# Kernel tuning notes

Measured on AMD Instinct MI355X. Metric: run time of the kernel, lower is better.

The kernel has to match this reference:

```python
import jax, jax.numpy as jnp
import numpy as np

N = 50000      # n_nodes
E = 800000     # n_edges
IN_NF = 64     # in_node_nf
HID = 128      # hidden_nf
OUT_NF = 64    # out_node_nf
L = 4          # n_layers
EH = HID // 2  # edge MLP hidden width (edge_nf_ratio=2)
C = 1.0        # aggregation scaling constant


def _w(k, shape):
    # fan-in scaled init (matches nn.Linear scale roughly)
    return jax.random.normal(k, shape, dtype=jnp.float32) / np.sqrt(shape[-2]).astype(np.float32)


def setup_inputs() -> dict:
    key = jax.random.key(0)
    ks = jax.random.split(key, 10)
    h = jax.random.normal(ks[0], (N, IN_NF), dtype=jnp.float32)
    edges = jax.random.randint(ks[1], (2, E), 0, N, dtype=jnp.int32)
    return {
        "h": h,
        "edges": edges,
        "W_in": _w(ks[2], (IN_NF, HID)),
        "b_in": jnp.zeros((HID,), jnp.float32),
        # stacked per-layer GCL params, leading dim L
        "eW1": _w(ks[3], (L, 2 * HID, EH)),
        "eb1": jnp.zeros((L, EH), jnp.float32),
        "eW2": _w(ks[4], (L, EH, EH)),
        "eb2": jnp.zeros((L, EH), jnp.float32),
        "nW1": _w(ks[5], (L, HID + EH, HID)),
        "nb1": jnp.zeros((L, HID), jnp.float32),
        "nW2": _w(ks[6], (L, HID, HID)),
        "nb2": jnp.zeros((L, HID), jnp.float32),
        "W_out": _w(ks[7], (HID, OUT_NF)),
        "b_out": jnp.zeros((OUT_NF,), jnp.float32),
    }


def reference(h, edges, W_in, b_in, eW1, eb1, eW2, eb2, nW1, nb1, nW2, nb2, W_out, b_out):
    row, col = edges[0], edges[1]
    h = h @ W_in + b_in  # [N, HID] embedding_in

    def layer(hc, p):
        w1, b1, w2, b2, m1, c1, m2, c2 = p
        # edge model: gather endpoints, concat, 2-layer SiLU MLP
        m = jnp.concatenate([hc[row], hc[col]], axis=1)          # [E, 2*HID]
        m = jax.nn.silu(m @ w1 + b1)                             # [E, EH]
        m = jax.nn.silu(m @ w2 + b2)                             # [E, EH]
        # node model: scatter-sum messages to source nodes, scale by C
        agg = jax.ops.segment_sum(m, row, num_segments=N) * C    # [N, EH]
        z = jnp.concatenate([hc, agg], axis=1)                   # [N, HID+EH]
        z = jax.nn.silu(z @ m1 + c1)
        z = z @ m2 + c2                                          # [N, HID]
        return hc + z, None  # residual=True

    h, _ = jax.lax.scan(layer, h, (eW1, eb1, eW2, eb2, nW1, nb1, nW2, nb2))
    return h @ W_out + b_out  # [N, OUT_NF] embedding_out
```

## Files before the change

### kernel.cpp

```cpp
#include <hip/hip_runtime.h>
#include <hip/hip_bf16.h>
#include <cstdint>
#include <cstddef>

#define N_NODES 50000
#define N_EDGES 800000
#define NR      50048
#define NBKT    196
#define BSH     8
#define BCHUNK  2048
#define CAP     6144

typedef __attribute__((ext_vector_type(8))) short short8;
typedef __attribute__((ext_vector_type(4))) float floatx4;
typedef __attribute__((ext_vector_type(4))) unsigned int uintx4;

__device__ inline float bf2f(unsigned short u) {
    union { unsigned int i; float f; } v; v.i = ((unsigned int)u) << 16; return v.f;
}
__device__ inline unsigned short f2bf(float f) {
    union { float f; unsigned int i; } v; v.f = f;
    unsigned int u = v.i;
    return (unsigned short)((u + 0x7FFFu + ((u >> 16) & 1u)) >> 16);
}
__device__ inline unsigned int f2bf_pk(float a, float b) {
    __hip_bfloat162 h2 = __float22bfloat162_rn(make_float2(a, b));
    return *reinterpret_cast<unsigned int*>(&h2);
}
__device__ inline float2 bf2f2(unsigned int u) {
    union { unsigned int i; float f; } lo, hi;
    lo.i = u << 16;
    hi.i = u & 0xFFFF0000u;
    return make_float2(lo.f, hi.f);
}
__device__ inline float silu_f(float x) {
    float e = __expf(-x);
    return x * __builtin_amdgcn_rcpf(1.0f + e);
}

__device__ inline int block_excl_scan_256(int v, int* buf) {
    int tid = threadIdx.x;
    buf[tid] = v;
    __syncthreads();
    #pragma unroll
    for (int off = 1; off < 256; off <<= 1) {
        int t = (tid >= off) ? buf[tid - off] : 0;
        __syncthreads();
        buf[tid] += t;
        __syncthreads();
    }
    return buf[tid] - v;
}

__device__ inline void pack_std(const float* __restrict__ src,
                                unsigned short* __restrict__ dst,
                                int NOUT, long j) {
    int i = (int)(j & 7);
    long rest = j >> 3;
    int n = (int)(rest % NOUT);
    int kb = (int)(rest / NOUT);
    dst[j] = f2bf(src[(long)(kb * 8 + i) * NOUT + n]);
}

#define NH0   (N_NODES * 64L)
#define SW_IN 8192L
#define SW_OUT 8192L
#define SW1   16384L
#define SE2   4096L
#define SN1   24576L
#define SN2   16384L
#define SB    128L
#define PERL  (SW1 + SE2 + SN1 + SN2 + SB)
#define PACK_TOTAL (NH0 + SW_IN + SW_OUT + 4 * PERL)

__global__ __launch_bounds__(256) void pack_kernel(
    const float* __restrict__ h0, const float* __restrict__ W_in,
    const float* __restrict__ W_out, const float* __restrict__ eW1,
    const float* __restrict__ eb1, const float* __restrict__ eW2,
    const float* __restrict__ nW1, const float* __restrict__ nW2,
    unsigned short* __restrict__ h0bf, unsigned short* __restrict__ Winp,
    unsigned short* __restrict__ Woutp, unsigned short* __restrict__ W1p,
    unsigned short* __restrict__ eW2p, unsigned short* __restrict__ nW1p,
    unsigned short* __restrict__ nW2p, float* __restrict__ biasP)
{
    long idx = (long)blockIdx.x * 256 + threadIdx.x;
    if (idx >= PACK_TOTAL) return;
    long j = idx;
    if (j < NH0) { h0bf[j] = f2bf(h0[j]); return; }
    j -= NH0;
    if (j < SW_IN) { pack_std(W_in, Winp, 128, j); return; }
    j -= SW_IN;
    if (j < SW_OUT) { pack_std(W_out, Woutp, 64, j); return; }
    j -= SW_OUT;
    int l = (int)(j / PERL);
    long r = j % PERL;
    if (r < SW1) {
        int i = (int)(r & 7);
        int n = (int)((r >> 3) & 127);
        int kb = (int)(r >> 10);
        int k = kb * 8 + i;
        const float* w = eW1 + (long)l * 256 * 64;
        float v = (n < 64) ? w[(long)k * 64 + n] : w[(long)(128 + k) * 64 + (n - 64)];
        W1p[(long)l * SW1 + r] = f2bf(v);
        return;
    }
    r -= SW1;
    if (r < SE2) { pack_std(eW2 + (long)l * 4096, eW2p + (long)l * SE2, 64, r); return; }
    r -= SE2;
    if (r < SN1) { pack_std(nW1 + (long)l * 24576, nW1p + (long)l * SN1, 128, r); return; }
    r -= SN1;
    if (r < SN2) { pack_std(nW2 + (long)l * 16384, nW2p + (long)l * SN2, 128, r); return; }
    r -= SN2;
    biasP[(long)l * 128 + r] = (r < 64) ? eb1[(long)l * 64 + r] : 0.0f;
}

__global__ __launch_bounds__(256) void hist_k(const int* __restrict__ erow,
                                              int* __restrict__ countB, int E) {
    __shared__ int c[NBKT];
    for (int i = threadIdx.x; i < NBKT; i += 256) c[i] = 0;
    __syncthreads();
    int j = blockIdx.x * BCHUNK + threadIdx.x;
    #pragma unroll
    for (int i = 0; i < BCHUNK / 256; i++, j += 256)
        if (j < E) atomicAdd(&c[erow[j] >> BSH], 1);
    __syncthreads();
    for (int i = threadIdx.x; i < NBKT; i += 256)
        if (c[i]) atomicAdd(&countB[i], c[i]);
}

__global__ __launch_bounds__(256) void bucket_scan_k(const int* __restrict__ countB,
                                                     int* __restrict__ bucketBase,
                                                     int* __restrict__ bucketCursor) {
    __shared__ int buf[256];
    int tid = threadIdx.x;
    int v = (tid < NBKT) ? countB[tid] : 0;
    int excl = block_excl_scan_256(v, buf);
    if (tid < NBKT) {
        bucketBase[tid] = excl;
        bucketCursor[tid] = excl;
    }
    if (tid == NBKT - 1) bucketBase[NBKT] = excl + v;
}

__global__ __launch_bounds__(256) void bin_k(
    const int* __restrict__ erow, const int* __restrict__ ecol,
    int* __restrict__ bucketCursor, int2* __restrict__ binned, int E)
{
    __shared__ int2 staged[BCHUNK];
    __shared__ int cnt[NBKT];
    __shared__ int binStart[NBKT];
    __shared__ int gbase[NBKT];
    __shared__ int scanbuf[256];
    const int tid = threadIdx.x;
    const int base = blockIdx.x * BCHUNK;
    const int nloc = min(BCHUNK, E - base);

    for (int i = tid; i < NBKT; i += 256) cnt[i] = 0;
    __syncthreads();

    int2 ed[BCHUNK / 256];
    int  bo[BCHUNK / 256];
    #pragma unroll
    for (int i = 0; i < BCHUNK / 256; i++) {
        int jl = i * 256 + tid;
        if (jl < nloc) {
            int j = base + jl;
            int r = erow[j], c = ecol[j];
            ed[i] = make_int2(r, c);
            int b = r >> BSH;
            int off = atomicAdd(&cnt[b], 1);
            bo[i] = (b << 12) | off;
        } else bo[i] = -1;
    }
    __syncthreads();

    int v = (tid < NBKT) ? cnt[tid] : 0;
    int excl = block_excl_scan_256(v, scanbuf);
    if (tid < NBKT) binStart[tid] = excl;
    if (tid < NBKT && v > 0) gbase[tid] = atomicAdd(&bucketCursor[tid], v);
    __syncthreads();

    #pragma unroll
    for (int i = 0; i < BCHUNK / 256; i++) {
        if (bo[i] >= 0)
            staged[binStart[bo[i] >> 12] + (bo[i] & 0xFFF)] = ed[i];
    }
    __syncthreads();

    for (int j = tid; j < nloc; j += 256) {
        int2 e = staged[j];
        int b = e.x >> BSH;
        binned[gbase[b] + (j - binStart[b])] = e;
    }
}

__global__ __launch_bounds__(256) void sort_k(
    const int2* __restrict__ binned, const int* __restrict__ bucketBase,
    int2* __restrict__ eidx)
{
    __shared__ int2 st[CAP];
    __shared__ int2 st2[CAP];
    __shared__ int cnt[256];
    __shared__ int cur[256];
    __shared__ int scanbuf[256];
    const int b = blockIdx.x;
    const int tid = threadIdx.x;
    const int s0 = bucketBase[b];
    int n = bucketBase[b + 1] - s0;
    if (n > CAP) n = CAP;

    cnt[tid] = 0;
    __syncthreads();
    for (int j = tid; j < n; j += 256) {
        int2 e = binned[s0 + j];
        st[j] = e;
        atomicAdd(&cnt[e.x & 255], 1);
    }
    __syncthreads();
    int excl = block_excl_scan_256(cnt[tid], scanbuf);
    cur[tid] = excl;
    __syncthreads();
    for (int j = tid; j < n; j += 256) {
        int2 e = st[j];
        int pos = atomicAdd(&cur[e.x & 255], 1);
        st2[pos] = e;
    }
    __syncthreads();
    for (int j = tid; j < n; j += 256)
        eidx[s0 + j] = st2[j];
}

__global__ __launch_bounds__(256) void edge_fused_k(
    const int2* __restrict__ eidx,
    const unsigned short* __restrict__ P,
    const unsigned short* __restrict__ Bp,
    const float* __restrict__ b2, float* __restrict__ agg, int E)
{
    __shared__ float M2s[64 * 68];
    __shared__ int ridS[64];
    __shared__ short segStartS[66];
    __shared__ int nsegS;
    const int tid = threadIdx.x;
    const int wave = tid >> 6;
    const int lane = tid & 63;
    const int lrow = lane & 15;
    const int quad = lane >> 4;
    const int e0 = blockIdx.x * 64;
    const int el = wave * 16 + lrow;
    const int e = e0 + el;

    short8 af0 = {0, 0, 0, 0, 0, 0, 0, 0};
    short8 af1 = af0;
    if (e < E) {
        int2 rc = eidx[e];
        int rr = rc.x, cc = rc.y;
        if (quad == 0) ridS[el] = rr;
        const uintx4* pt = (const uintx4*)(P + (size_t)rr * 128 + quad * 8);
        const uintx4* pb = (const uintx4*)(P + (size_t)cc * 128 + 64 + quad * 8);
        uintx4 t0 = pt[0], t1 = pt[4];
        uintx4 b0 = pb[0], b1 = pb[4];
        const unsigned int* t0u = (const unsigned int*)&t0;
        const unsigned int* t1u = (const unsigned int*)&t1;
        const unsigned int* b0u = (const unsigned int*)&b0;
        const unsigned int* b1u = (const unsigned int*)&b1;
        unsigned int o0[4], o1[4];
        #pragma unroll
        for (int i = 0; i < 4; i++) {
            float2 a0 = bf2f2(t0u[i]), c0 = bf2f2(b0u[i]);
            o0[i] = f2bf_pk(silu_f(a0.x + c0.x), silu_f(a0.y + c0.y));
            float2 a1 = bf2f2(t1u[i]), c1 = bf2f2(b1u[i]);
            o1[i] = f2bf_pk(silu_f(a1.x + c1.x), silu_f(a1.y + c1.y));
        }
        af0 = *(const short8*)o0;
        af1 = *(const short8*)o1;
    } else if (quad == 0) {
        ridS[el] = -1;
    }

    floatx4 acc[4];
    #pragma unroll
    for (int i = 0; i < 4; i++) acc[i] = (floatx4){0, 0, 0, 0};
    #pragma unroll
    for (int nt = 0; nt < 4; nt++) {
        short8 bf0 = *(const short8*)(Bp + (size_t)((0 * 4 + quad) * 64 + nt * 16 + lrow) * 8);
        acc[nt] = __builtin_amdgcn_mfma_f32_16x16x32_bf16(af0, bf0, acc[nt], 0, 0, 0);
        short8 bf1 = *(const short8*)(Bp + (size_t)((1 * 4 + quad) * 64 + nt * 16 + lrow) * 8);
        acc[nt] = __builtin_amdgcn_mfma_f32_16x16x32_bf16(af1, bf1, acc[nt], 0, 0, 0);
    }

    #pragma unroll
    for (int nt = 0; nt < 4; nt++) {
        int n = nt * 16 + lrow;
        float bv = b2[n];
        #pragma unroll
        for (int r = 0; r < 4; r++) {
            int el2 = wave * 16 + quad * 4 + r;
            M2s[el2 * 68 + n] = silu_f(acc[nt][r] + bv);
        }
    }
    __syncthreads();

    if (tid < 64) {
        bool st = (ridS[tid] >= 0) && (tid == 0 || ridS[tid] != ridS[tid - 1]);
        unsigned long long m = __ballot(st);
        if (st) {
            int pos = __popcll(m & ((1ull << tid) - 1));
            segStartS[pos] = (short)tid;
        }
        if (tid == 0) {
            int ns = __popcll(m);
            nsegS = ns;
            int nvalid = E - e0;
            if (nvalid > 64) nvalid = 64;
            segStartS[ns] = (short)nvalid;
        }
    }
    __syncthreads();

    {
        int f = tid & 63;
        int g = tid >> 6;
        int ns = nsegS;
        for (int j = g; j < ns; j += 4) {
            int a = segStartS[j], b = segStartS[j + 1];
            float s = 0.0f;
            for (int el2 = a; el2 < b; el2++) s += M2s[el2 * 68 + f];
            int rv = ridS[a];
            if (j == 0 || j == ns - 1)
                atomicAdd(&agg[(size_t)rv * 64 + f], s);
            else
                agg[(size_t)rv * 64 + f] = s;
        }
    }
}

#define SROW 336
template<int FINAL>
__global__ __launch_bounds__(512) void node_fused_k(
    const unsigned short* __restrict__ hbf, const float* __restrict__ agg,
    const unsigned short* __restrict__ W1, const float* __restrict__ b1,
    const unsigned short* __restrict__ W2, const float* __restrict__ b2,
    const unsigned short* __restrict__ B3, const float* __restrict__ bias3,
    float* __restrict__ hFT, unsigned short* __restrict__ hB,
    unsigned short* __restrict__ Pout, float* __restrict__ outF,
    float* __restrict__ aggZ, int M)
{
    __shared__ unsigned short S[64 * SROW];
    const int tid = threadIdx.x;
    const int m0 = blockIdx.x * 64;
    const int wave = tid >> 6;
    const int lane = tid & 63;
    const int lrow = lane & 15;
    const int quad = lane >> 4;
    const int g = wave >> 1;
    const int h = wave & 1;
    const int row0 = m0 + g * 16 + quad * 4;
    const int elb = g * 16 + quad * 4;

    floatx4 res4[4];
    #pragma unroll
    for (int j = 0; j < 4; j++) {
        int n = (4 * h + j) * 16 + lrow;
        res4[j] = *(const floatx4*)(hFT + (size_t)n * NR + row0);
    }

    for (int t = tid; t < 64 * 24; t += 512) {
        int rr = t / 24, c = t % 24;
        int row = m0 + rr;
        uintx4 val = {0, 0, 0, 0};
        if (row < M) {
            if (c < 16) {
                val = *(const uintx4*)(hbf + (size_t)row * 128 + c * 8);
            } else {
                const floatx4* s4 = (const floatx4*)(agg + (size_t)row * 64 + (c - 16) * 8);
                floatx4 f0 = s4[0], f1 = s4[1];
                unsigned int tmp[4];
                tmp[0] = f2bf_pk(f0[0], f0[1]);
                tmp[1] = f2bf_pk(f0[2], f0[3]);
                tmp[2] = f2bf_pk(f1[0], f1[1]);
                tmp[3] = f2bf_pk(f1[2], f1[3]);
                val = *(const uintx4*)tmp;
            }
        }
        *(uintx4*)(&S[rr * SROW + c * 8]) = val;
    }
    __syncthreads();

    if (!FINAL) {
        floatx4 z = {0, 0, 0, 0};
        for (int t = tid; t < 64 * 16; t += 512) {
            int rr = t >> 4, c = t & 15;
            int row = m0 + rr;
            if (row < M) *(floatx4*)(aggZ + (size_t)row * 64 + c * 4) = z;
        }
    }

    const unsigned short* arow = &S[(g * 16 + lrow) * SROW];

    floatx4 acc[4];
    #pragma unroll
    for (int i = 0; i < 4; i++) acc[i] = (floatx4){0, 0, 0, 0};
    #pragma unroll
    for (int kt = 0; kt < 6; kt++) {
        short8 afrag = *(const short8*)(arow + kt * 32 + quad * 8);
        int kb = kt * 4 + quad;
        #pragma unroll
        for (int j = 0; j < 4; j++) {
            int n = (4 * h + j) * 16 + lrow;
            short8 bfrag = *(const short8*)(W1 + (size_t)(kb * 128 + n) * 8);
            acc[j] = __builtin_amdgcn_mfma_f32_16x16x32_bf16(afrag, bfrag, acc[j], 0, 0, 0);
        }
    }

    #pragma unroll
    for (int j = 0; j < 4; j++) {
        int n = (4 * h + j) * 16 + lrow;
        float bv = b1[n];
        unsigned int p01 = f2bf_pk(silu_f(acc[j][0] + bv), silu_f(acc[j][1] + bv));
        unsigned int p23 = f2bf_pk(silu_f(acc[j][2] + bv), silu_f(acc[j][3] + bv));
        S[(elb + 0) * SROW + 192 + n] = (unsigned short)(p01 & 0xFFFF);
        S[(elb + 1) * SROW + 192 + n] = (unsigned short)(p01 >> 16);
        S[(elb + 2) * SROW + 192 + n] = (unsigned short)(p23 & 0xFFFF);
        S[(elb + 3) * SROW + 192 + n] = (unsigned short)(p23 >> 16);
    }
    __syncthreads();

    floatx4 acc2[4];
    #pragma unroll
    for (int i = 0; i < 4; i++) acc2[i] = (floatx4){0, 0, 0, 0};
    #pragma unroll
    for (int kt = 0; kt < 4; kt++) {
        short8 afrag = *(const short8*)(arow + 192 + kt * 32 + quad * 8);
        int kb = kt * 4 + quad;
        #pragma unroll
        for (int j = 0; j < 4; j++) {
            int n = (4 * h + j) * 16 + lrow;
            short8 bfrag = *(const short8*)(W2 + (size_t)(kb * 128 + n) * 8);
            acc2[j] = __builtin_amdgcn_mfma_f32_16x16x32_bf16(afrag, bfrag, acc2[j], 0, 0, 0);
        }
    }

    #pragma unroll
    for (int j = 0; j < 4; j++) {
        int n = (4 * h + j) * 16 + lrow;
        float bv = b2[n];
        floatx4 v4;
        #pragma unroll
        for (int r = 0; r < 4; r++) v4[r] = acc2[j][r] + bv + res4[j][r];
        unsigned int p01 = f2bf_pk(v4[0], v4[1]);
        unsigned int p23 = f2bf_pk(v4[2], v4[3]);
        S[(elb + 0) * SROW + n] = (unsigned short)(p01 & 0xFFFF);
        S[(elb + 1) * SROW + n] = (unsigned short)(p01 >> 16);
        S[(elb + 2) * SROW + n] = (unsigned short)(p23 & 0xFFFF);
        S[(elb + 3) * SROW + n] = (unsigned short)(p23 >> 16);
        if (!FINAL && row0 < M)
            *(floatx4*)(hFT + (size_t)n * NR + row0) = v4;
    }
    __syncthreads();

    constexpr int NT3 = FINAL ? 2 : 4;
    constexpr int NO3 = FINAL ? 64 : 128;
    floatx4 acc3[NT3];
    #pragma unroll
    for (int i = 0; i < NT3; i++) acc3[i] = (floatx4){0, 0, 0, 0};
    #pragma unroll
    for (int kt = 0; kt < 4; kt++) {
        short8 afrag = *(const short8*)(arow + kt * 32 + quad * 8);
        int kb = kt * 4 + quad;
        #pragma unroll
        for (int j = 0; j < NT3; j++) {
            int n = (NT3 * h + j) * 16 + lrow;
            short8 bfrag = *(const short8*)(B3 + (size_t)(kb * NO3 + n) * 8);
            acc3[j] = __builtin_amdgcn_mfma_f32_16x16x32_bf16(afrag, bfrag, acc3[j], 0, 0, 0);
        }
    }
    #pragma unroll
    for (int j = 0; j < NT3; j++) {
        int n = (NT3 * h + j) * 16 + lrow;
        float bv = bias3[n];
        if (FINAL) {
            #pragma unroll
            for (int r = 0; r < 4; r++)
                ((float*)(&S[(elb + r) * SROW + 128]))[n] = acc3[j][r] + bv;
        } else {
            unsigned int p01 = f2bf_pk(acc3[j][0] + bv, acc3[j][1] + bv);
            unsigned int p23 = f2bf_pk(acc3[j][2] + bv, acc3[j][3] + bv);
            S[(elb + 0) * SROW + 128 + n] = (unsigned short)(p01 & 0xFFFF);
            S[(elb + 1) * SROW + 128 + n] = (unsigned short)(p01 >> 16);
            S[(elb + 2) * SROW + 128 + n] = (unsigned short)(p23 & 0xFFFF);
            S[(elb + 3) * SROW + 128 + n] = (unsigned short)(p23 >> 16);
        }
    }
    __syncthreads();

    if (FINAL) {
        for (int t = tid; t < 64 * 16; t += 512) {
            int rr = t >> 4, c = t & 15;
            int row = m0 + rr;
            if (row < M)
                *(floatx4*)(outF + (size_t)row * 64 + c * 4) =
                    *(const floatx4*)((const float*)(&S[rr * SROW + 128]) + c * 4);
        }
    } else {
        for (int t = tid; t < 64 * 32; t += 512) {
            int rr = t >> 5, c = t & 31;
            int row = m0 + rr;
            if (row < M) {
                if (c < 16)
                    *(uintx4*)(hB + (size_t)row * 128 + c * 8) =
                        *(const uintx4*)(&S[rr * SROW + c * 8]);
                else
                    *(uintx4*)(Pout + (size_t)row * 128 + (c - 16) * 8) =
                        *(const uintx4*)(&S[rr * SROW + 128 + (c - 16) * 8]);
            }
        }
    }
}

#define SROWE 264
__global__ __launch_bounds__(256) void embed_fused_k(
    const unsigned short* __restrict__ h0bf, const unsigned short* __restrict__ Win,
    const float* __restrict__ b_in, const unsigned short* __restrict__ W1,
    const float* __restrict__ biasP, float* __restrict__ hFT,
    unsigned short* __restrict__ hB, unsigned short* __restrict__ Pout, int M)
{
    __shared__ unsigned short S[64 * SROWE];
    const int tid = threadIdx.x;
    const int m0 = blockIdx.x * 64;
    const int wave = tid >> 6;
    const int lane = tid & 63;
    const int lrow = lane & 15;
    const int quad = lane >> 4;
    const int row0 = m0 + wave * 16 + quad * 4;
    const int elb = wave * 16 + quad * 4;

    for (int t = tid; t < 64 * 8; t += 256) {
        int rr = t >> 3, c = t & 7;
        int row = m0 + rr;
        uintx4 val = {0, 0, 0, 0};
        if (row < M) val = *(const uintx4*)(h0bf + (size_t)row * 64 + c * 8);
        *(uintx4*)(&S[rr * SROWE + c * 8]) = val;
    }
    __syncthreads();

    const unsigned short* arow = &S[(wave * 16 + lrow) * SROWE];

    floatx4 acc[8];
    #pragma unroll
    for (int i = 0; i < 8; i++) acc[i] = (floatx4){0, 0, 0, 0};
    #pragma unroll
    for (int kt = 0; kt < 2; kt++) {
        short8 afrag = *(const short8*)(arow + kt * 32 + quad * 8);
        int kb = kt * 4 + quad;
        #pragma unroll
        for (int nt = 0; nt < 8; nt++) {
            short8 bfrag = *(const short8*)(Win + (size_t)(kb * 128 + nt * 16 + lrow) * 8);
            acc[nt] = __builtin_amdgcn_mfma_f32_16x16x32_bf16(afrag, bfrag, acc[nt], 0, 0, 0);
        }
    }

    #pragma unroll
    for (int nt = 0; nt < 8; nt++) {
        int n = nt * 16 + lrow;
        float bv = b_in[n];
        floatx4 v4;
        #pragma unroll
        for (int r = 0; r < 4; r++) v4[r] = acc[nt][r] + bv;
        unsigned int p01 = f2bf_pk(v4[0], v4[1]);
        unsigned int p23 = f2bf_pk(v4[2], v4[3]);
        S[(elb + 0) * SROWE + n] = (unsigned short)(p01 & 0xFFFF);
        S[(elb + 1) * SROWE + n] = (unsigned short)(p01 >> 16);
        S[(elb + 2) * SROWE + n] = (unsigned short)(p23 & 0xFFFF);
        S[(elb + 3) * SROWE + n] = (unsigned short)(p23 >> 16);
        if (row0 < M)
            *(floatx4*)(hFT + (size_t)n * NR + row0) = v4;
    }

    floatx4 acc3[8];
    #pragma unroll
    for (int i = 0; i < 8; i++) acc3[i] = (floatx4){0, 0, 0, 0};
    #pragma unroll
    for (int kt = 0; kt < 4; kt++) {
        short8 afrag = *(const short8*)(arow + kt * 32 + quad * 8);
        int kb = kt * 4 + quad;
        #pragma unroll
        for (int nt = 0; nt < 8; nt++) {
            short8 bfrag = *(const short8*)(W1 + (size_t)(kb * 128 + nt * 16 + lrow) * 8);
            acc3[nt] = __builtin_amdgcn_mfma_f32_16x16x32_bf16(afrag, bfrag, acc3[nt], 0, 0, 0);
        }
    }
    #pragma unroll
    for (int nt = 0; nt < 8; nt++) {
        int n = nt * 16 + lrow;
        float bv = biasP[n];
        unsigned int p01 = f2bf_pk(acc3[nt][0] + bv, acc3[nt][1] + bv);
        unsigned int p23 = f2bf_pk(acc3[nt][2] + bv, acc3[nt][3] + bv);
        S[(elb + 0) * SROWE + 128 + n] = (unsigned short)(p01 & 0xFFFF);
        S[(elb + 1) * SROWE + 128 + n] = (unsigned short)(p01 >> 16);
        S[(elb + 2) * SROWE + 128 + n] = (unsigned short)(p23 & 0xFFFF);
        S[(elb + 3) * SROWE + 128 + n] = (unsigned short)(p23 >> 16);
    }
    __syncthreads();

    for (int t = tid; t < 64 * 32; t += 256) {
        int rr = t / 32, c = t % 32;
        int row = m0 + rr;
        if (row < M) {
            if (c < 16)
                *(uintx4*)(hB + (size_t)row * 128 + c * 8) =
                    *(const uintx4*)(&S[rr * SROWE + c * 8]);
            else
                *(uintx4*)(Pout + (size_t)row * 128 + (c - 16) * 8) =
                    *(const uintx4*)(&S[rr * SROWE + 128 + (c - 16) * 8]);
        }
    }
}

extern "C" void kernel_launch(void* const* d_in, const int* in_sizes, int n_in,
                              void* d_out, int out_size, void* d_ws, size_t ws_size,
                              hipStream_t stream) {
    const float* h0   = (const float*)d_in[0];
    const int*   edges= (const int*)d_in[1];
    const float* W_in = (const float*)d_in[2];
    const float* b_in = (const float*)d_in[3];
    const float* eW1  = (const float*)d_in[4];
    const float* eb1  = (const float*)d_in[5];
    const float* eW2  = (const float*)d_in[6];
    const float* eb2  = (const float*)d_in[7];
    const float* nW1  = (const float*)d_in[8];
    const float* nb1  = (const float*)d_in[9];
    const float* nW2  = (const float*)d_in[10];
    const float* nb2  = (const float*)d_in[11];
    const float* W_out= (const float*)d_in[12];
    const float* b_out= (const float*)d_in[13];
    float* out = (float*)d_out;

    const int E = in_sizes[1] / 2;
    const int* erow = edges;
    const int* ecol = edges + E;

    char* ws = (char*)d_ws;
    unsigned short* hbf  = (unsigned short*)(ws + 0);
    float*          hFT  = (float*)(ws + 12800000);
    unsigned short* P    = (unsigned short*)(ws + 38424576);
    float*          agg  = (float*)(ws + 51224576);
    int2*           binned=(int2*)(ws + 51224576);
    unsigned short* h0bf = (unsigned short*)(ws + 76824576);
    int2*           eidx = (int2*)(ws + 76824576);
    float*          biasP= (float*)(ws + 83224576);
    unsigned short* Winp = (unsigned short*)(ws + 83226624);
    unsigned short* Woutp= (unsigned short*)(ws + 83243008);
    unsigned short* W1p  = (unsigned short*)(ws + 83259392);
    unsigned short* eW2p = (unsigned short*)(ws + 83390464);
    unsigned short* nW1p = (unsigned short*)(ws + 83423232);
    unsigned short* nW2p = (unsigned short*)(ws + 83619840);
    int*            countB=(int*)(ws + 83750912);
    int*            bucketBase=(int*)(ws + 83751936);
    int*            bucketCursor=(int*)(ws + 83752960);

    const int gemm_grid = (N_NODES + 63) / 64;
    const int edge_grid = (E + 63) / 64;
    const int pack_grid = (int)((PACK_TOTAL + 255) / 256);
    const int bin_grid  = (E + BCHUNK - 1) / BCHUNK;

    hipMemsetAsync(countB, 0, NBKT * 4, stream);
    pack_kernel<<<pack_grid, 256, 0, stream>>>(h0, W_in, W_out, eW1, eb1, eW2,
                                               nW1, nW2, h0bf, Winp, Woutp, W1p,
                                               eW2p, nW1p, nW2p, biasP);

    hist_k<<<bin_grid, 256, 0, stream>>>(erow, countB, E);
    bucket_scan_k<<<1, 256, 0, stream>>>(countB, bucketBase, bucketCursor);
    bin_k<<<bin_grid, 256, 0, stream>>>(erow, ecol, bucketCursor, binned, E);

    embed_fused_k<<<gemm_grid, 256, 0, stream>>>(
        h0bf, Winp, b_in, W1p, biasP, hFT, hbf, P, N_NODES);

    sort_k<<<NBKT, 256, 0, stream>>>(binned, bucketBase, eidx);

    hipMemsetAsync(agg, 0, (size_t)N_NODES * 64 * 4, stream);

    for (int l = 0; l < 4; l++) {
        edge_fused_k<<<edge_grid, 256, 0, stream>>>(
            eidx, P, eW2p + (size_t)l * SE2, eb2 + (size_t)l * 64, agg, E);
        if (l < 3) {
            node_fused_k<0><<<gemm_grid, 512, 0, stream>>>(
                hbf, agg, nW1p + (size_t)l * SN1, nb1 + (size_t)l * 128,
                nW2p + (size_t)l * SN2, nb2 + (size_t)l * 128,
                W1p + (size_t)(l + 1) * SW1, biasP + (size_t)(l + 1) * 128,
                hFT, hbf, P, nullptr, agg, N_NODES);
        } else {
            node_fused_k<1><<<gemm_grid, 512, 0, stream>>>(
                hbf, agg, nW1p + (size_t)l * SN1, nb1 + (size_t)l * 128,
                nW2p + (size_t)l * SN2, nb2 + (size_t)l * 128,
                Woutp, b_out, hFT, hbf, nullptr, out, nullptr, N_NODES);
        }
    }
}
```

Before: 436.9 us.

## Load agg fragments directly into registers and scatter sorted edges straight to global

The node kernel now reads aggregated messages from global memory straight into MFMA A-fragments, converting to bf16 in registers instead of staging them through shared memory. This shrinks the shared tile row stride and lets launch bounds request higher occupancy. The bucket sort writes each edge directly to its final global slot, dropping the second shared buffer and a barrier but giving up coalesced global writes. The new agg loads have no row<M guard, so the last partial block may read past N rows into padding.

```diff
diff --git a/kernel.cpp b/kernel.cpp
--- a/kernel.cpp
+++ b/kernel.cpp
@@ -199,7 +199,6 @@
     int2* __restrict__ eidx)
 {
     __shared__ int2 st[CAP];
-    __shared__ int2 st2[CAP];
     __shared__ int cnt[256];
     __shared__ int cur[256];
     __shared__ int scanbuf[256];
@@ -223,11 +222,8 @@
     for (int j = tid; j < n; j += 256) {
         int2 e = st[j];
         int pos = atomicAdd(&cur[e.x & 255], 1);
-        st2[pos] = e;
-    }
-    __syncthreads();
-    for (int j = tid; j < n; j += 256)
-        eidx[s0 + j] = st2[j];
+        eidx[s0 + pos] = e;
+    }
 }
 
 __global__ __launch_bounds__(256) void edge_fused_k(
@@ -334,9 +330,9 @@
     }
 }
 
-#define SROW 336
+#define SROW 264
 template<int FINAL>
-__global__ __launch_bounds__(512) void node_fused_k(
+__global__ __launch_bounds__(512, 8) void node_fused_k(
     const unsigned short* __restrict__ hbf, const float* __restrict__ agg,
     const unsigned short* __restrict__ W1, const float* __restrict__ b1,
     const unsigned short* __restrict__ W2, const float* __restrict__ b2,
@@ -357,6 +353,21 @@
     const int row0 = m0 + g * 16 + quad * 4;
     const int elb = g * 16 + quad * 4;
 
+    short8 afa0, afa1;
+    {
+        const float* ap = agg + (size_t)(m0 + g * 16 + lrow) * 64;
+        floatx4 q0 = *(const floatx4*)(ap + quad * 8);
+        floatx4 q1 = *(const floatx4*)(ap + quad * 8 + 4);
+        floatx4 q2 = *(const floatx4*)(ap + 32 + quad * 8);
+        floatx4 q3 = *(const floatx4*)(ap + 32 + quad * 8 + 4);
+        unsigned int c0[4] = { f2bf_pk(q0[0], q0[1]), f2bf_pk(q0[2], q0[3]),
+                               f2bf_pk(q1[0], q1[1]), f2bf_pk(q1[2], q1[3]) };
+        unsigned int c1[4] = { f2bf_pk(q2[0], q2[1]), f2bf_pk(q2[2], q2[3]),
+                               f2bf_pk(q3[0], q3[1]), f2bf_pk(q3[2], q3[3]) };
+        afa0 = *(const short8*)c0;
+        afa1 = *(const short8*)c1;
+    }
+
     floatx4 res4[4];
     #pragma unroll
     for (int j = 0; j < 4; j++) {
@@ -364,24 +375,11 @@
         res4[j] = *(const floatx4*)(hFT + (size_t)n * NR + row0);
     }
 
-    for (int t = tid; t < 64 * 24; t += 512) {
-        int rr = t / 24, c = t % 24;
+    for (int t = tid; t < 64 * 16; t += 512) {
+        int rr = t >> 4, c = t & 15;
         int row = m0 + rr;
         uintx4 val = {0, 0, 0, 0};
-        if (row < M) {
-            if (c < 16) {
-                val = *(const uintx4*)(hbf + (size_t)row * 128 + c * 8);
-            } else {
-                const floatx4* s4 = (const floatx4*)(agg + (size_t)row * 64 + (c - 16) * 8);
-                floatx4 f0 = s4[0], f1 = s4[1];
-                unsigned int tmp[4];
-                tmp[0] = f2bf_pk(f0[0], f0[1]);
-                tmp[1] = f2bf_pk(f0[2], f0[3]);
-                tmp[2] = f2bf_pk(f1[0], f1[1]);
-                tmp[3] = f2bf_pk(f1[2], f1[3]);
-                val = *(const uintx4*)tmp;
-            }
-        }
+        if (row < M) val = *(const uintx4*)(hbf + (size_t)row * 128 + c * 8);
         *(uintx4*)(&S[rr * SROW + c * 8]) = val;
     }
     __syncthreads();
@@ -401,7 +399,7 @@
     #pragma unroll
     for (int i = 0; i < 4; i++) acc[i] = (floatx4){0, 0, 0, 0};
     #pragma unroll
-    for (int kt = 0; kt < 6; kt++) {
+    for (int kt = 0; kt < 4; kt++) {
         short8 afrag = *(const short8*)(arow + kt * 32 + quad * 8);
         int kb = kt * 4 + quad;
         #pragma unroll
@@ -410,6 +408,14 @@
             short8 bfrag = *(const short8*)(W1 + (size_t)(kb * 128 + n) * 8);
             acc[j] = __builtin_amdgcn_mfma_f32_16x16x32_bf16(afrag, bfrag, acc[j], 0, 0, 0);
         }
+    }
+    #pragma unroll
+    for (int j = 0; j < 4; j++) {
+        int n = (4 * h + j) * 16 + lrow;
+        short8 b4 = *(const short8*)(W1 + (size_t)((16 + quad) * 128 + n) * 8);
+        acc[j] = __builtin_amdgcn_mfma_f32_16x16x32_bf16(afa0, b4, acc[j], 0, 0, 0);
+        short8 b5 = *(const short8*)(W1 + (size_t)((20 + quad) * 128 + n) * 8);
+        acc[j] = __builtin_amdgcn_mfma_f32_16x16x32_bf16(afa1, b5, acc[j], 0, 0, 0);
     }
 
     #pragma unroll
@@ -418,10 +424,10 @@
         float bv = b1[n];
         unsigned int p01 = f2bf_pk(silu_f(acc[j][0] + bv), silu_f(acc[j][1] + bv));
         unsigned int p23 = f2bf_pk(silu_f(acc[j][2] + bv), silu_f(acc[j][3] + bv));
-        S[(elb + 0) * SROW + 192 + n] = (unsigned short)(p01 & 0xFFFF);
-        S[(elb + 1) * SROW + 192 + n] = (unsigned short)(p01 >> 16);
-        S[(elb + 2) * SROW + 192 + n] = (unsigned short)(p23 & 0xFFFF);
-        S[(elb + 3) * SROW + 192 + n] = (unsigned short)(p23 >> 16);
+        S[(elb + 0) * SROW + 128 + n] = (unsigned short)(p01 & 0xFFFF);
+        S[(elb + 1) * SROW + 128 + n] = (unsigned short)(p01 >> 16);
+        S[(elb + 2) * SROW + 128 + n] = (unsigned short)(p23 & 0xFFFF);
+        S[(elb + 3) * SROW + 128 + n] = (unsigned short)(p23 >> 16);
     }
     __syncthreads();
 
@@ -430,7 +436,7 @@
     for (int i = 0; i < 4; i++) acc2[i] = (floatx4){0, 0, 0, 0};
     #pragma unroll
     for (int kt = 0; kt < 4; kt++) {
-        short8 afrag = *(const short8*)(arow + 192 + kt * 32 + quad * 8);
+        short8 afrag = *(const short8*)(arow + 128 + kt * 32 + quad * 8);
         int kb = kt * 4 + quad;
         #pragma unroll
         for (int j = 0; j < 4; j++) {
```

New measurement: 463.0 us. 1.06x slower.
